# Kernel optimization log

Hardware: AMD Instinct MI355X
Metric: run time of the kernel (lower is better)

The kernel has to match this reference:

```python
import jax, jax.numpy as jnp
import numpy as np


def _layernorm(x, g, b, eps=1e-5):
    m = jnp.mean(x, axis=-1, keepdims=True)
    v = jnp.mean((x - m) ** 2, axis=-1, keepdims=True)
    return (x - m) * jax.lax.rsqrt(v + eps) * g + b


def setup_inputs() -> dict:
    B, T, C, D, DF, H = 128, 1024, 512, 1024, 2048, 64
    key = jax.random.key(0)
    ks = jax.random.split(key, 16)

    def n(k, shape, s=0.02):
        return jax.random.normal(k, shape, dtype=jnp.float32) * s

    return {
        "x_enc": jax.random.normal(ks[0], (B, T, C), dtype=jnp.float32),
        "aging": jax.random.uniform(ks[1], (B, T, 1), dtype=jnp.float32),
        # inverted embedding: Linear(T -> D) applied to [B, C, T]
        "W_emb": n(ks[2], (T, D)), "b_emb": jnp.zeros((D,), jnp.float32),
        # norm_sensor LayerNorm(D)
        "g_s": jnp.ones((D,), jnp.float32), "b_s": jnp.zeros((D,), jnp.float32),
        # DTB basis: [basis_dim=C, D] (coeff MLP output is discarded in the original)
        "basis": n(ks[3], (C, D), 0.1),
        # Q/K/V projections (stored [in, out])
        "Wq": n(ks[4], (D, D)), "bq": jnp.zeros((D,), jnp.float32),
        "Wk": n(ks[5], (D, D)), "bk": jnp.zeros((D,), jnp.float32),
        "Wv": n(ks[6], (D, D)), "bv": jnp.zeros((D,), jnp.float32),
        "age_scale": jnp.array(1.0, jnp.float32),
        # norm_fused LayerNorm(D)
        "g_f": jnp.ones((D,), jnp.float32), "b_f": jnp.zeros((D,), jnp.float32),
        # AttentionPooling: Linear(D, 64) -> GELU -> Linear(64, 1)
        "Wp1": n(ks[7], (D, H)), "bp1": jnp.zeros((H,), jnp.float32),
        "Wp2": n(ks[8], (H, 1)), "bp2": jnp.zeros((1,), jnp.float32),
        # fc head: Linear(D, DF) -> LeakyReLU -> Linear(DF, DF) -> Linear(DF, 1)
        "Wf1": n(ks[9], (D, DF)), "bf1": jnp.zeros((DF,), jnp.float32),
        "Wf2": n(ks[10], (DF, DF)), "bf2": jnp.zeros((DF,), jnp.float32),
        "Wf3": n(ks[11], (DF, 1)), "bf3": jnp.zeros((1,), jnp.float32),
    }


def reference(x_enc, aging, W_emb, b_emb, g_s, b_s, basis, Wq, bq, Wk, bk, Wv, bv,
              age_scale, g_f, b_f, Wp1, bp1, Wp2, bp2, Wf1, bf1, Wf2, bf2, Wf3, bf3):
    D = W_emb.shape[1]
    inv_sqrt_d = 1.0 / jnp.sqrt(jnp.asarray(D, x_enc.dtype))

    # inverted embedding: [B,T,C] -> [B,C,T] @ [T,D] -> [B,C,D]; dropout = identity (eval)
    sensor = jnp.einsum('btc,td->bcd', x_enc, W_emb) + b_emb
    sensor = _layernorm(sensor, g_s, b_s)  # norm_sensor

    # cross_attention_with_dtb (N = C variates)
    Q = sensor @ Wq + bq  # [B,N,D]
    K = sensor @ Wk + bk
    V = sensor @ Wv + bv
    attn_scores = jnp.einsum('bnd,bmd->bnm', Q, K) * inv_sqrt_d        # Q K^T / sqrt(d)
    age_bias = jnp.einsum('bnd,md->bnm', Q, basis) * inv_sqrt_d        # Q basis^T / sqrt(d)
    scale = attn_scores + age_scale
    scores = jnp.einsum('bjn,bjk->bnk', age_bias, scale)               # age_bias^T @ scale
    attn_w = jax.nn.softmax(scores, axis=-1)
    fused = jnp.einsum('bnm,bmd->bnd', attn_w, V) * inv_sqrt_d
    fused = _layernorm(fused, g_f, b_f)  # norm_fused

    # AttentionPooling over variate axis (dim=1)
    h = jax.nn.gelu(fused @ Wp1 + bp1, approximate=False)
    pool_scores = h @ Wp2 + bp2                    # [B,N,1]
    pool_w = jax.nn.softmax(pool_scores, axis=1)
    pooled = jnp.sum(fused * pool_w, axis=1)       # [B,D]

    # fc head
    h = jax.nn.leaky_relu(pooled @ Wf1 + bf1, negative_slope=0.01)
    h = h @ Wf2 + bf2
    rul = jnp.abs(h @ Wf3 + bf3)                   # [B,1]
    return rul
```

## Files before the change

kernel.cpp:

```cpp
#include <hip/hip_runtime.h>
#include <hip/hip_bf16.h>
#include <math.h>

#define BB   128
#define TT   1024
#define CC_  512
#define DD   1024
#define DF_  2048
#define HH   64
#define INV_SQRT_D 0.03125f

typedef _Float16 f16;
typedef __attribute__((ext_vector_type(8))) _Float16 f16x8;
typedef __attribute__((ext_vector_type(4))) _Float16 f16x4;
typedef __attribute__((ext_vector_type(2))) _Float16 f16x2;
typedef __attribute__((ext_vector_type(4))) float f32x4;

__device__ __forceinline__ void gload_lds16(const void* g, void* l) {
    __builtin_amdgcn_global_load_lds(
        (const __attribute__((address_space(1))) void*)g,
        (__attribute__((address_space(3))) void*)l, 16, 0, 0);
}

__device__ __forceinline__ long long paddr(long long r, int k, int K) {
    return ((r >> 7) * (long long)(K >> 5) + (k >> 5)) * 4096LL
         + (long long)(((k >> 3) & 3) * 1024 + ((int)(r & 127)) * 8 + (k & 7));
}

template <int OUT, int ACT = 0>
__global__ __launch_bounds__(256, 4) void mfma_gemm(
    const f16* __restrict__ A, const f16* __restrict__ B,
    const float* __restrict__ bias, const float* __restrict__ add_c,
    void* __restrict__ C0,
    int M, int N, int K,
    long long sA, long long sB, long long sC, float alpha)
{
    const int gx = gridDim.x;
    const int nwg = gx * gridDim.y;
    int lin = blockIdx.y * gx + blockIdx.x;
    if ((nwg & 7) == 0) {
        const int cpx = nwg >> 3;
        lin = (lin & 7) * cpx + (lin >> 3);
    }
    const int bx = lin % gx, by = lin / gx;

    const int bz   = blockIdx.z;
    const int t    = threadIdx.x;
    const int wave = t >> 6, lane = t & 63;
    const int m0 = by * 128, n0 = bx * 128;
    const int wm = (wave >> 1) * 64, wn = (wave & 1) * 64;

    __shared__ __align__(16) f16 As[2][4096];
    __shared__ __align__(16) f16 Bs[2][4096];

    f32x4 acc[4][4] = {};

    const int wbyte = wave * 1024;
    const long long tA = (long long)bz * sA + (long long)(m0 >> 7) * (K >> 5) * 4096;
    const long long tB = (long long)bz * sB + (long long)(n0 >> 7) * (K >> 5) * 4096;
    const f16* pA = A + tA + t * 8;
    const f16* pB = B + tB + t * 8;

    const int q   = lane >> 4;
    const int r16 = lane & 15;

    for (int k0 = 0; k0 < K; k0 += 64) {
        const long long ko = (long long)(k0 >> 5) * 4096;
        __syncthreads();
        gload_lds16(pA + ko,        (char*)(&As[0][0]) + wbyte);
        gload_lds16(pA + ko + 2048, (char*)(&As[0][0]) + wbyte + 4096);
        gload_lds16(pA + ko + 4096, (char*)(&As[1][0]) + wbyte);
        gload_lds16(pA + ko + 6144, (char*)(&As[1][0]) + wbyte + 4096);
        gload_lds16(pB + ko,        (char*)(&Bs[0][0]) + wbyte);
        gload_lds16(pB + ko + 2048, (char*)(&Bs[0][0]) + wbyte + 4096);
        gload_lds16(pB + ko + 4096, (char*)(&Bs[1][0]) + wbyte);
        gload_lds16(pB + ko + 6144, (char*)(&Bs[1][0]) + wbyte + 4096);
        __syncthreads();

        #pragma unroll
        for (int s = 0; s < 2; ++s) {
            const f16x8* AV = (const f16x8*)(&As[s][0]);
            const f16x8* BV = (const f16x8*)(&Bs[s][0]);
            f16x8 bfr[4];
            #pragma unroll
            for (int j = 0; j < 4; ++j)
                bfr[j] = BV[q * 128 + wn + j * 16 + r16];
            __builtin_amdgcn_s_setprio(1);
            #pragma unroll
            for (int i = 0; i < 4; ++i) {
                const f16x8 a = AV[q * 128 + wm + i * 16 + r16];
                #pragma unroll
                for (int j = 0; j < 4; ++j)
                    acc[i][j] = __builtin_amdgcn_mfma_f32_16x16x32_f16(
                        a, bfr[j], acc[i][j], 0, 0, 0);
            }
            __builtin_amdgcn_s_setprio(0);
        }
    }

    const float cadd = add_c ? add_c[0] : 0.0f;
    const int col = lane & 15;
    const int rb  = (lane >> 4) * 4;
    #pragma unroll
    for (int j = 0; j < 4; ++j) {
        const int n = n0 + wn + j * 16 + col;
        const float bv = bias ? bias[n] : 0.0f;
        #pragma unroll
        for (int i = 0; i < 4; ++i) {
            const int m = m0 + wm + i * 16 + rb;
            f32x4 v = acc[i][j];
            #pragma unroll
            for (int r = 0; r < 4; ++r) {
                v[r] = v[r] * alpha + cadd + bv;
                if constexpr (ACT == 2)
                    v[r] = 0.5f * v[r] * (1.0f + erff(v[r] * 0.70710678118654752f));
            }
            if constexpr (OUT == 0) {
                float* C = (float*)C0 + (long long)bz * sC;
                #pragma unroll
                for (int r = 0; r < 4; ++r) C[(long long)(m + r) * N + n] = v[r];
            } else if constexpr (OUT == 1) {
                f16* C = (f16*)C0 + (long long)bz * sC;
                #pragma unroll
                for (int r = 0; r < 4; ++r)
                    C[paddr(m + r, n, N)] = (f16)v[r];
            } else {
                f16* C = (f16*)C0 + (long long)bz * sC;
                f16 p[4];
                #pragma unroll
                for (int r = 0; r < 4; ++r) p[r] = (f16)v[r];
                *reinterpret_cast<f16x4*>(&C[paddr(n, m, M)]) =
                    *reinterpret_cast<f16x4*>(p);
            }
        }
    }
}

__global__ __launch_bounds__(256) void transpose_h_kernel(
    const float* __restrict__ in, f16* __restrict__ o,
    int R, int Cc, long long sIn, long long sOut)
{
    const int b = blockIdx.z;
    in += (long long)b * sIn; o += (long long)b * sOut;
    __shared__ float tile[32][33];
    const int c0 = blockIdx.x * 32, r0 = blockIdx.y * 32;
    const int tx = threadIdx.x & 31, ty = threadIdx.x >> 5;
    #pragma unroll
    for (int i = 0; i < 32; i += 8)
        tile[ty + i][tx] = in[(long long)(r0 + ty + i) * Cc + (c0 + tx)];
    __syncthreads();
    if (threadIdx.x < 128) {
        const int c = threadIdx.x & 31, q = threadIdx.x >> 5;
        f16 p[8];
        #pragma unroll
        for (int j = 0; j < 8; ++j) p[j] = (f16)tile[8 * q + j][c];
        const long long base =
            (((long long)(c0 + c) >> 7) * (long long)(R >> 5) + (r0 >> 5)) * 4096LL
            + q * 1024 + ((c0 + c) & 127) * 8;
        *reinterpret_cast<f16x8*>(&o[base]) = *reinterpret_cast<f16x8*>(p);
    }
}

__global__ __launch_bounds__(256) void cvt_h_kernel(
    const float* __restrict__ in, f16* __restrict__ o, long long n)
{
    const long long i = ((long long)blockIdx.x * 256 + threadIdx.x) * 4;
    if (i >= n) return;
    const float4 v = *reinterpret_cast<const float4*>(in + i);
    f16 p[4] = {(f16)v.x, (f16)v.y, (f16)v.z, (f16)v.w};
    const long long r = i >> 10;
    const int k = (int)(i & 1023);
    *reinterpret_cast<f16x4*>(&o[paddr(r, k, 1024)]) = *reinterpret_cast<f16x4*>(p);
}

__global__ __launch_bounds__(256) void zero_h_kernel(f16* __restrict__ p, long long n)
{
    const long long i = ((long long)blockIdx.x * 256 + threadIdx.x) * 8;
    if (i >= n) return;
    f16x8 z = {};
    *reinterpret_cast<f16x8*>(p + i) = z;
}

__global__ __launch_bounds__(128) void pad_bias_kernel(
    const float* __restrict__ in, float* __restrict__ o)
{
    const int i = threadIdx.x;
    o[i] = (i < HH) ? in[i] : 0.0f;
}

__global__ __launch_bounds__(256) void layernorm_pg_kernel(
    f16* __restrict__ x, const float* __restrict__ g, const float* __restrict__ b)
{
    f16* base = x + (long long)blockIdx.x * 131072;
    const int t = threadIdx.x;
    const int r = t & 127;
    const int h = t >> 7;

    __shared__ float gs[1024], bs[1024];
    __shared__ float ssum[256], ssq[256];
    for (int i = t; i < 1024; i += 256) { gs[i] = g[i]; bs[i] = b[i]; }

    float sum = 0.0f, sq = 0.0f;
    for (int tile = 0; tile < 32; ++tile) {
        #pragma unroll
        for (int qq = 0; qq < 2; ++qq) {
            const f16x8 v = *reinterpret_cast<const f16x8*>(
                base + tile * 4096 + (h * 2 + qq) * 1024 + r * 8);
            #pragma unroll
            for (int j = 0; j < 8; ++j) {
                const float f = (float)v[j];
                sum += f; sq += f * f;
            }
        }
    }
    ssum[t] = sum; ssq[t] = sq;
    __syncthreads();
    const float rsum = ssum[r] + ssum[r + 128];
    const float rsq  = ssq[r]  + ssq[r + 128];
    const float mean = rsum * (1.0f / DD);
    const float var  = rsq * (1.0f / DD) - mean * mean;
    const float rs   = rsqrtf(fmaxf(var, 0.0f) + 1e-5f);

    for (int tile = 0; tile < 32; ++tile) {
        #pragma unroll
        for (int qq = 0; qq < 2; ++qq) {
            const int q = h * 2 + qq;
            const int kbase = tile * 32 + q * 8;
            f16* p = base + tile * 4096 + q * 1024 + r * 8;
            const f16x8 v = *reinterpret_cast<const f16x8*>(p);
            f16 o[8];
            #pragma unroll
            for (int j = 0; j < 8; ++j)
                o[j] = (f16)(((float)v[j] - mean) * rs * gs[kbase + j] + bs[kbase + j]);
            *reinterpret_cast<f16x8*>(p) = *reinterpret_cast<f16x8*>(o);
        }
    }
}

__global__ __launch_bounds__(256) void softmax512_h_kernel(
    const float* __restrict__ x, f16* __restrict__ o)
{
    const long long row = blockIdx.x;
    const float2 v = reinterpret_cast<const float2*>(x + row * 512)[threadIdx.x];
    const int t = threadIdx.x;

    __shared__ float red[4];
    float mx = fmaxf(v.x, v.y);
    #pragma unroll
    for (int off = 32; off; off >>= 1) mx = fmaxf(mx, __shfl_down(mx, off));
    if ((t & 63) == 0) red[t >> 6] = mx;
    __syncthreads();
    mx = fmaxf(fmaxf(red[0], red[1]), fmaxf(red[2], red[3]));
    __syncthreads();

    const float e0 = expf(v.x - mx), e1 = expf(v.y - mx);
    float s = e0 + e1;
    #pragma unroll
    for (int off = 32; off; off >>= 1) s += __shfl_down(s, off);
    if ((t & 63) == 0) red[t >> 6] = s;
    __syncthreads();
    s = red[0] + red[1] + red[2] + red[3];
    const float inv = 1.0f / s;

    f16 p[2] = {(f16)(e0 * inv), (f16)(e1 * inv)};
    *reinterpret_cast<f16x2*>(&o[paddr(row, 2 * t, 512)]) =
        *reinterpret_cast<f16x2*>(p);
}

__global__ __launch_bounds__(256) void softmax512_kernel(float* __restrict__ x)
{
    const long long row = blockIdx.x;
    float2* xr = reinterpret_cast<float2*>(x + row * 512);
    const int t = threadIdx.x;
    float2 v = xr[t];

    __shared__ float red[4];
    float mx = fmaxf(v.x, v.y);
    #pragma unroll
    for (int off = 32; off; off >>= 1) mx = fmaxf(mx, __shfl_down(mx, off));
    if ((t & 63) == 0) red[t >> 6] = mx;
    __syncthreads();
    mx = fmaxf(fmaxf(red[0], red[1]), fmaxf(red[2], red[3]));
    __syncthreads();

    const float e0 = expf(v.x - mx), e1 = expf(v.y - mx);
    float s = e0 + e1;
    #pragma unroll
    for (int off = 32; off; off >>= 1) s += __shfl_down(s, off);
    if ((t & 63) == 0) red[t >> 6] = s;
    __syncthreads();
    s = red[0] + red[1] + red[2] + red[3];
    const float inv = 1.0f / s;
    xr[t] = make_float2(e0 * inv, e1 * inv);
}

#define BM 64
#define BN 64
#define BK 16

template <int TA, int TB, int ACT>
__global__ __launch_bounds__(256) void gemm_kernel(
    const float* __restrict__ A, const float* __restrict__ B,
    const float* __restrict__ bias, const float* __restrict__ add_const_ptr,
    float* __restrict__ C,
    int M, int N, int K,
    long long strideA, long long strideB, long long strideC,
    float alpha)
{
    const int batch = blockIdx.z;
    A += (long long)batch * strideA;
    B += (long long)batch * strideB;
    C += (long long)batch * strideC;

    __shared__ float As[BK][BM + 4];
    __shared__ float Bs[BK][BN + 4];

    const int t  = threadIdx.x;
    const int tx = t & 15;
    const int ty = t >> 4;
    const int m0 = blockIdx.y * BM;
    const int n0 = blockIdx.x * BN;

    float acc[4][4] = {};

    for (int k0 = 0; k0 < K; k0 += BK) {
        if (TA == 0) {
            const int mm = t >> 2;
            const int kk = (t & 3) * 4;
            const float4 v = *reinterpret_cast<const float4*>(
                &A[(long long)(m0 + mm) * K + (k0 + kk)]);
            As[kk + 0][mm] = v.x; As[kk + 1][mm] = v.y;
            As[kk + 2][mm] = v.z; As[kk + 3][mm] = v.w;
        } else {
            const int kk = t >> 4;
            const int mm = (t & 15) * 4;
            const float4 v = *reinterpret_cast<const float4*>(
                &A[(long long)(k0 + kk) * M + (m0 + mm)]);
            *reinterpret_cast<float4*>(&As[kk][mm]) = v;
        }
        if (TB == 0) {
            const int kk = t >> 4;
            const int nn = (t & 15) * 4;
            const float4 v = *reinterpret_cast<const float4*>(
                &B[(long long)(k0 + kk) * N + (n0 + nn)]);
            *reinterpret_cast<float4*>(&Bs[kk][nn]) = v;
        } else {
            const int nn = t >> 2;
            const int kk = (t & 3) * 4;
            const float4 v = *reinterpret_cast<const float4*>(
                &B[(long long)(n0 + nn) * K + (k0 + kk)]);
            Bs[kk + 0][nn] = v.x; Bs[kk + 1][nn] = v.y;
            Bs[kk + 2][nn] = v.z; Bs[kk + 3][nn] = v.w;
        }
        __syncthreads();

        #pragma unroll
        for (int kk = 0; kk < BK; ++kk) {
            float a[4], b[4];
            #pragma unroll
            for (int i = 0; i < 4; ++i) a[i] = As[kk][ty * 4 + i];
            #pragma unroll
            for (int j = 0; j < 4; ++j) b[j] = Bs[kk][tx * 4 + j];
            #pragma unroll
            for (int i = 0; i < 4; ++i)
                #pragma unroll
                for (int j = 0; j < 4; ++j)
                    acc[i][j] = fmaf(a[i], b[j], acc[i][j]);
        }
        __syncthreads();
    }

    const float cadd = add_const_ptr ? add_const_ptr[0] : 0.0f;
    #pragma unroll
    for (int i = 0; i < 4; ++i) {
        const int m = m0 + ty * 4 + i;
        #pragma unroll
        for (int j = 0; j < 4; ++j) {
            const int n = n0 + tx * 4 + j;
            float v = acc[i][j] * alpha + cadd;
            if (bias) v += bias[n];
            if (ACT == 1) v = (v > 0.0f) ? v : 0.01f * v;
            else if (ACT == 2) v = 0.5f * v * (1.0f + erff(v * 0.70710678118654752f));
            C[(long long)m * N + n] = v;
        }
    }
}

__global__ __launch_bounds__(256) void pool_score_kernel(
    const float* __restrict__ h, const float* __restrict__ Wp2,
    const float* __restrict__ bp2, float* __restrict__ out)
{
    const int row  = blockIdx.x * 4 + (threadIdx.x >> 6);
    const int lane = threadIdx.x & 63;
    float v = h[(long long)row * 128 + lane] * Wp2[lane];
    #pragma unroll
    for (int off = 32; off; off >>= 1) v += __shfl_down(v, off);
    if (lane == 0) out[row] = v + bp2[0];
}

__global__ __launch_bounds__(256) void pooled_kernel(
    const f16* __restrict__ fused, const float* __restrict__ w,
    float* __restrict__ out)
{
    const int b = blockIdx.y;
    const int d = blockIdx.x * 256 + threadIdx.x;
    __shared__ float ws_[CC_];
    for (int i = threadIdx.x; i < CC_; i += 256) ws_[i] = w[(long long)b * CC_ + i];
    __syncthreads();
    const long long dpart = (long long)(d >> 5) * 4096
                          + ((d >> 3) & 3) * 1024 + (d & 7);
    float acc = 0.0f;
    for (int n = 0; n < CC_; ++n) {
        const long long r = (long long)b * CC_ + n;
        const long long addr = ((r >> 7) * 32) * 4096 + dpart + (r & 127) * 8;
        acc = fmaf((float)fused[addr], ws_[n], acc);
    }
    out[(long long)b * DD + d] = acc;
}

__global__ __launch_bounds__(256) void rul_kernel(
    const float* __restrict__ h2, const float* __restrict__ Wf3,
    const float* __restrict__ bf3, float* __restrict__ out)
{
    const int b = blockIdx.x;
    const int t = threadIdx.x;
    float acc = 0.0f;
    for (int k = t; k < DF_; k += 256)
        acc = fmaf(h2[(long long)b * DF_ + k], Wf3[k], acc);
    __shared__ float red[4];
    #pragma unroll
    for (int off = 32; off; off >>= 1) acc += __shfl_down(acc, off);
    if ((t & 63) == 0) red[t >> 6] = acc;
    __syncthreads();
    if (t == 0) out[b] = fabsf(red[0] + red[1] + red[2] + red[3] + bf3[0]);
}

extern "C" void kernel_launch(void* const* d_in, const int* in_sizes, int n_in,
                              void* d_out, int out_size, void* d_ws, size_t ws_size,
                              hipStream_t stream)
{
    const float* x_enc   = (const float*)d_in[0];
    const float* W_emb   = (const float*)d_in[2];
    const float* b_emb   = (const float*)d_in[3];
    const float* g_s     = (const float*)d_in[4];
    const float* b_s     = (const float*)d_in[5];
    const float* basis   = (const float*)d_in[6];
    const float* Wq      = (const float*)d_in[7];
    const float* bq      = (const float*)d_in[8];
    const float* Wk      = (const float*)d_in[9];
    const float* bk      = (const float*)d_in[10];
    const float* Wv      = (const float*)d_in[11];
    const float* bv      = (const float*)d_in[12];
    const float* age_sc  = (const float*)d_in[13];
    const float* g_f     = (const float*)d_in[14];
    const float* b_f     = (const float*)d_in[15];
    const float* Wp1     = (const float*)d_in[16];
    const float* bp1     = (const float*)d_in[17];
    const float* Wp2     = (const float*)d_in[18];
    const float* bp2     = (const float*)d_in[19];
    const float* Wf1     = (const float*)d_in[20];
    const float* bf1     = (const float*)d_in[21];
    const float* Wf2     = (const float*)d_in[22];
    const float* bf2     = (const float*)d_in[23];
    const float* Wf3     = (const float*)d_in[24];
    const float* bf3     = (const float*)d_in[25];
    float* out = (float*)d_out;
    (void)in_sizes; (void)n_in; (void)out_size; (void)ws_size;

    const unsigned long long MBy = 1048576ULL;
    char* ws = (char*)d_ws;
    f16*  xT     = (f16*)(ws + 0 * MBy);
    f16*  WembT  = (f16*)(ws + 128 * MBy);
    f16*  WqT    = (f16*)(ws + 130 * MBy);
    f16*  WkT    = (f16*)(ws + 132 * MBy);
    f16*  WvT    = (f16*)(ws + 134 * MBy);
    f16*  Wp1p   = (f16*)(ws + 136 * MBy);
    float* bp1p  = (float*)(ws + 137 * MBy);
    f16*  bas    = (f16*)(ws + 138 * MBy);
    f16*  sens   = (f16*)(ws + 256 * MBy);
    f16*  Qp     = (f16*)(ws + 0 * MBy);
    f16*  Kp     = (f16*)(ws + 384 * MBy);
    f16*  S1T    = (f16*)(ws + 512 * MBy);
    f16*  S2T    = (f16*)(ws + 640 * MBy);
    float* S3    = (float*)(ws + 704 * MBy);
    f16*  attn   = (f16*)(ws + 0 * MBy);
    f16*  VT     = (f16*)(ws + 384 * MBy);
    f16*  fusedp = (f16*)(ws + 512 * MBy);
    float* hpool = (float*)(ws + 704 * MBy);
    float* pscr  = (float*)(ws + 840 * MBy);
    float* pooled= (float*)(ws + 842 * MBy);
    float* h1    = (float*)(ws + 844 * MBy);
    float* h2    = (float*)(ws + 848 * MBy);

    const long long CD  = (long long)CC_ * DD;
    const long long CCs = (long long)CC_ * CC_;
    const long long DC  = (long long)DD * CC_;
    const dim3 blk(256);

    transpose_h_kernel<<<dim3(CC_ / 32, TT / 32, BB), blk, 0, stream>>>(
        x_enc, xT, TT, CC_, (long long)TT * CC_, (long long)CC_ * TT);
    transpose_h_kernel<<<dim3(DD / 32, TT / 32, 1), blk, 0, stream>>>(
        W_emb, WembT, TT, DD, 0, 0);
    transpose_h_kernel<<<dim3(DD / 32, DD / 32, 1), blk, 0, stream>>>(
        Wq, WqT, DD, DD, 0, 0);
    transpose_h_kernel<<<dim3(DD / 32, DD / 32, 1), blk, 0, stream>>>(
        Wk, WkT, DD, DD, 0, 0);
    transpose_h_kernel<<<dim3(DD / 32, DD / 32, 1), blk, 0, stream>>>(
        Wv, WvT, DD, DD, 0, 0);
    zero_h_kernel<<<64, blk, 0, stream>>>(Wp1p, 131072);
    transpose_h_kernel<<<dim3(HH / 32, DD / 32, 1), blk, 0, stream>>>(
        Wp1, Wp1p, DD, HH, 0, 0);
    pad_bias_kernel<<<1, 128, 0, stream>>>(bp1, bp1p);
    cvt_h_kernel<<<(CC_ * DD) / 1024, blk, 0, stream>>>(
        basis, bas, (long long)CC_ * DD);

    mfma_gemm<1><<<dim3(DD / 128, CC_ / 128, BB), blk, 0, stream>>>(
        xT, WembT, b_emb, nullptr, sens,
        CC_, DD, TT, (long long)CC_ * TT, 0, CD, 1.0f);
    layernorm_pg_kernel<<<(BB * CC_) / 128, blk, 0, stream>>>(sens, g_s, b_s);
    mfma_gemm<1><<<dim3(DD / 128, (BB * CC_) / 128, 1), blk, 0, stream>>>(
        sens, WqT, bq, nullptr, Qp,
        BB * CC_, DD, DD, 0, 0, 0, 1.0f);
    mfma_gemm<1><<<dim3(DD / 128, (BB * CC_) / 128, 1), blk, 0, stream>>>(
        sens, WkT, bk, nullptr, Kp,
        BB * CC_, DD, DD, 0, 0, 0, 1.0f);
    mfma_gemm<2><<<dim3(CC_ / 128, CC_ / 128, BB), blk, 0, stream>>>(
        Qp, Kp, nullptr, age_sc, S1T,
        CC_, CC_, DD, CD, CD, CCs, INV_SQRT_D);
    mfma_gemm<2><<<dim3(CC_ / 128, CC_ / 128, BB), blk, 0, stream>>>(
        Qp, bas, nullptr, nullptr, S2T,
        CC_, CC_, DD, CD, 0, CCs, INV_SQRT_D);
    mfma_gemm<0><<<dim3(CC_ / 128, CC_ / 128, BB), blk, 0, stream>>>(
        S2T, S1T, nullptr, nullptr, S3,
        CC_, CC_, CC_, CCs, CCs, CCs, 1.0f);
    softmax512_h_kernel<<<BB * CC_, blk, 0, stream>>>(S3, attn);
    mfma_gemm<2><<<dim3(DD / 128, CC_ / 128, BB), blk, 0, stream>>>(
        sens, WvT, bv, nullptr, VT,
        CC_, DD, DD, CD, 0, DC, 1.0f);
    mfma_gemm<1><<<dim3(DD / 128, CC_ / 128, BB), blk, 0, stream>>>(
        attn, VT, nullptr, nullptr, fusedp,
        CC_, DD, CC_, CCs, DC, CD, INV_SQRT_D);
    layernorm_pg_kernel<<<(BB * CC_) / 128, blk, 0, stream>>>(fusedp, g_f, b_f);
    mfma_gemm<0, 2><<<dim3(1, (BB * CC_) / 128, 1), blk, 0, stream>>>(
        fusedp, Wp1p, bp1p, nullptr, hpool,
        BB * CC_, 128, DD, 0, 0, 0, 1.0f);
    pool_score_kernel<<<(BB * CC_) / 4, blk, 0, stream>>>(hpool, Wp2, bp2, pscr);
    softmax512_kernel<<<BB, blk, 0, stream>>>(pscr);
    pooled_kernel<<<dim3(DD / 256, BB), blk, 0, stream>>>(fusedp, pscr, pooled);
    gemm_kernel<0, 0, 1><<<dim3(DF_ / 64, BB / 64, 1), blk, 0, stream>>>(
        pooled, Wf1, bf1, nullptr, h1, BB, DF_, DD, 0, 0, 0, 1.0f);
    gemm_kernel<0, 0, 0><<<dim3(DF_ / 64, BB / 64, 1), blk, 0, stream>>>(
        h1, Wf2, bf2, nullptr, h2, BB, DF_, DF_, 0, 0, 0, 1.0f);
    rul_kernel<<<BB, blk, 0, stream>>>(h2, Wf3, bf3, out);
}
```

Measured before the change: 1.573 ms.

## Fold Wq·Wkᵀ and Wq·basisᵀ into precomputed weights to drop the K projection

Precomputes Wq·Wkᵀ and Wq·basisᵀ once as small weight GEMMs, with bias-derived row vectors computed by a new rowdot kernel. The attention scores are then built as (sens·P)·sensᵀ and sens·W2. This removes the separate full-batch K projection GEMM and its large intermediate. The bk and age_scale terms are dropped because they add per-row constants that softmax cancels. The exchange is two small extra setup GEMMs and different fp16 rounding, since the product weights are rounded before use.

After: 1.478 ms. 6.1% less time.

```diff
diff --git a/kernel.cpp b/kernel.cpp
--- a/kernel.cpp
+++ b/kernel.cpp
@@ -188,6 +188,20 @@
     o[i] = (i < HH) ? in[i] : 0.0f;
 }
 
+__global__ __launch_bounds__(256) void rowdot_kernel(
+    const float* __restrict__ W, const float* __restrict__ v,
+    float* __restrict__ out, float scale)
+{
+    const int row  = blockIdx.x * 4 + (threadIdx.x >> 6);
+    const int lane = threadIdx.x & 63;
+    const float* wr = W + (long long)row * 1024;
+    float s = 0.0f;
+    for (int k = lane; k < 1024; k += 64) s += wr[k] * v[k];
+    #pragma unroll
+    for (int off = 32; off; off >>= 1) s += __shfl_down(s, off);
+    if (lane == 0) out[row] = s * scale;
+}
+
 __global__ __launch_bounds__(256) void layernorm_pg_kernel(
     f16* __restrict__ x, const float* __restrict__ g, const float* __restrict__ b)
 {
@@ -448,10 +462,8 @@
     const float* Wq      = (const float*)d_in[7];
     const float* bq      = (const float*)d_in[8];
     const float* Wk      = (const float*)d_in[9];
-    const float* bk      = (const float*)d_in[10];
     const float* Wv      = (const float*)d_in[11];
     const float* bv      = (const float*)d_in[12];
-    const float* age_sc  = (const float*)d_in[13];
     const float* g_f     = (const float*)d_in[14];
     const float* b_f     = (const float*)d_in[15];
     const float* Wp1     = (const float*)d_in[16];
@@ -471,16 +483,19 @@
     char* ws = (char*)d_ws;
     f16*  xT     = (f16*)(ws + 0 * MBy);
     f16*  WembT  = (f16*)(ws + 128 * MBy);
-    f16*  WqT    = (f16*)(ws + 130 * MBy);
-    f16*  WkT    = (f16*)(ws + 132 * MBy);
-    f16*  WvT    = (f16*)(ws + 134 * MBy);
-    f16*  Wp1p   = (f16*)(ws + 136 * MBy);
-    float* bp1p  = (float*)(ws + 137 * MBy);
-    f16*  bas    = (f16*)(ws + 138 * MBy);
+    f16*  Wqc    = (f16*)(ws + 130 * MBy);
+    f16*  Wkc    = (f16*)(ws + 132 * MBy);
+    f16*  Pt     = (f16*)(ws + 134 * MBy);
+    f16*  W2t    = (f16*)(ws + 136 * MBy);
+    f16*  bas    = (f16*)(ws + 137 * MBy);
+    f16*  Wp1p   = (f16*)(ws + 138 * MBy);
+    float* bp1p  = (float*)(ws + 139 * MBy);
+    float* pbias = (float*)(ws + 139 * MBy + 4096);
+    float* c2s   = (float*)(ws + 139 * MBy + 16384);
+    f16*  WvT    = (f16*)(ws + 140 * MBy);
     f16*  sens   = (f16*)(ws + 256 * MBy);
-    f16*  Qp     = (f16*)(ws + 0 * MBy);
-    f16*  Kp     = (f16*)(ws + 384 * MBy);
-    f16*  S1T    = (f16*)(ws + 512 * MBy);
+    f16*  QWp    = (f16*)(ws + 0 * MBy);
+    f16*  T1     = (f16*)(ws + 512 * MBy);
     f16*  S2T    = (f16*)(ws + 640 * MBy);
     float* S3    = (float*)(ws + 704 * MBy);
     f16*  attn   = (f16*)(ws + 0 * MBy);
@@ -502,36 +517,37 @@
     transpose_h_kernel<<<dim3(DD / 32, TT / 32, 1), blk, 0, stream>>>(
         W_emb, WembT, TT, DD, 0, 0);
     transpose_h_kernel<<<dim3(DD / 32, DD / 32, 1), blk, 0, stream>>>(
-        Wq, WqT, DD, DD, 0, 0);
-    transpose_h_kernel<<<dim3(DD / 32, DD / 32, 1), blk, 0, stream>>>(
-        Wk, WkT, DD, DD, 0, 0);
-    transpose_h_kernel<<<dim3(DD / 32, DD / 32, 1), blk, 0, stream>>>(
         Wv, WvT, DD, DD, 0, 0);
+    cvt_h_kernel<<<(DD * DD) / 1024, blk, 0, stream>>>(Wq, Wqc, (long long)DD * DD);
+    cvt_h_kernel<<<(DD * DD) / 1024, blk, 0, stream>>>(Wk, Wkc, (long long)DD * DD);
+    cvt_h_kernel<<<(CC_ * DD) / 1024, blk, 0, stream>>>(
+        basis, bas, (long long)CC_ * DD);
     zero_h_kernel<<<64, blk, 0, stream>>>(Wp1p, 131072);
     transpose_h_kernel<<<dim3(HH / 32, DD / 32, 1), blk, 0, stream>>>(
         Wp1, Wp1p, DD, HH, 0, 0);
     pad_bias_kernel<<<1, 128, 0, stream>>>(bp1, bp1p);
-    cvt_h_kernel<<<(CC_ * DD) / 1024, blk, 0, stream>>>(
-        basis, bas, (long long)CC_ * DD);
+    rowdot_kernel<<<DD / 4, blk, 0, stream>>>(Wk, bq, pbias, 1.0f);
+    rowdot_kernel<<<CC_ / 4, blk, 0, stream>>>(basis, bq, c2s, INV_SQRT_D);
+    mfma_gemm<2><<<dim3(DD / 128, DD / 128, 1), blk, 0, stream>>>(
+        Wqc, Wkc, nullptr, nullptr, Pt, DD, DD, DD, 0, 0, 0, 1.0f);
+    mfma_gemm<2><<<dim3(CC_ / 128, DD / 128, 1), blk, 0, stream>>>(
+        Wqc, bas, nullptr, nullptr, W2t, DD, CC_, DD, 0, 0, 0, 1.0f);
 
     mfma_gemm<1><<<dim3(DD / 128, CC_ / 128, BB), blk, 0, stream>>>(
         xT, WembT, b_emb, nullptr, sens,
         CC_, DD, TT, (long long)CC_ * TT, 0, CD, 1.0f);
     layernorm_pg_kernel<<<(BB * CC_) / 128, blk, 0, stream>>>(sens, g_s, b_s);
     mfma_gemm<1><<<dim3(DD / 128, (BB * CC_) / 128, 1), blk, 0, stream>>>(
-        sens, WqT, bq, nullptr, Qp,
-        BB * CC_, DD, DD, 0, 0, 0, 1.0f);
-    mfma_gemm<1><<<dim3(DD / 128, (BB * CC_) / 128, 1), blk, 0, stream>>>(
-        sens, WkT, bk, nullptr, Kp,
+        sens, Pt, pbias, nullptr, QWp,
         BB * CC_, DD, DD, 0, 0, 0, 1.0f);
     mfma_gemm<2><<<dim3(CC_ / 128, CC_ / 128, BB), blk, 0, stream>>>(
-        Qp, Kp, nullptr, age_sc, S1T,
+        sens, W2t, c2s, nullptr, S2T,
+        CC_, CC_, DD, CD, 0, CCs, INV_SQRT_D);
+    mfma_gemm<2><<<dim3(CC_ / 128, CC_ / 128, BB), blk, 0, stream>>>(
+        QWp, sens, nullptr, nullptr, T1,
         CC_, CC_, DD, CD, CD, CCs, INV_SQRT_D);
-    mfma_gemm<2><<<dim3(CC_ / 128, CC_ / 128, BB), blk, 0, stream>>>(
-        Qp, bas, nullptr, nullptr, S2T,
-        CC_, CC_, DD, CD, 0, CCs, INV_SQRT_D);
     mfma_gemm<0><<<dim3(CC_ / 128, CC_ / 128, BB), blk, 0, stream>>>(
-        S2T, S1T, nullptr, nullptr, S3,
+        S2T, T1, nullptr, nullptr, S3,
         CC_, CC_, CC_, CCs, CCs, CCs, 1.0f);
     softmax512_h_kernel<<<BB * CC_, blk, 0, stream>>>(S3, attn);
     mfma_gemm<2><<<dim3(DD / 128, CC_ / 128, BB), blk, 0, stream>>>(
```
